# Kernel optimization log

Hardware: AMD Instinct MI355X
Metric: run time of the kernel (lower is better)

Reference implementation:

```python
import jax, jax.numpy as jnp
import numpy as np

B, N, E = 32, 1024, 16384
F_IN, H, C = 4, 4, 64
HC = H * C          # 256, concat head dim
FC0, FC1 = 128, 1
NEG_SLOPE = 0.2


def setup_inputs() -> dict:
    key = jax.random.key(0)
    ks = jax.random.split(key, 20)
    x = jax.random.normal(ks[0], (B, N, F_IN), dtype=jnp.float32)
    e = jax.random.normal(ks[1], (B, E, 1), dtype=jnp.float32)  # ignored by GATConv (edge_dim=None)
    edge_index0 = jax.random.randint(ks[2], (2, E), 0, N, dtype=jnp.int64)
    edge_index1 = jax.random.randint(ks[3], (2, E), 0, N, dtype=jnp.int64)

    def glorot(k, shape):
        fan = shape[0] + shape[-1]
        return jax.random.uniform(k, shape, jnp.float32, -1.0, 1.0) * np.sqrt(6.0 / fan)

    # GAT layer 0: F_IN -> (H, C)
    W0 = glorot(ks[4], (F_IN, HC))
    att_src0 = glorot(ks[5], (H, C))
    att_dst0 = glorot(ks[6], (H, C))
    b0 = jnp.zeros((HC,), jnp.float32)
    # GAT layer 1: HC -> (H, C)
    W1 = glorot(ks[7], (HC, HC))
    att_src1 = glorot(ks[8], (H, C))
    att_dst1 = glorot(ks[9], (H, C))
    b1 = jnp.zeros((HC,), jnp.float32)
    # FC head: 256 -> 128 -> ReLU -> 1 (no final ReLU: duplicate 'ReLU' module name)
    fc0_w = glorot(ks[10], (HC, FC0))
    fc0_b = jnp.zeros((FC0,), jnp.float32)
    fc1_w = glorot(ks[11], (FC0, FC1))
    fc1_b = jnp.zeros((FC1,), jnp.float32)
    return dict(x=x, e=e, edge_index0=edge_index0, edge_index1=edge_index1,
                W0=W0, att_src0=att_src0, att_dst0=att_dst0, b0=b0,
                W1=W1, att_src1=att_src1, att_dst1=att_dst1, b1=b1,
                fc0_w=fc0_w, fc0_b=fc0_b, fc1_w=fc1_w, fc1_b=fc1_b)


def _segment_softmax(logits, seg, num_segments):
    # softmax over edges grouped by target node, per head
    m = jax.ops.segment_max(logits, seg, num_segments=num_segments)
    m = jnp.where(jnp.isfinite(m), m, 0.0)
    ex = jnp.exp(logits - m[seg])
    s = jax.ops.segment_sum(ex, seg, num_segments=num_segments)
    return ex / (s[seg] + 1e-16)


def _gat_layer(xi, edge_index, W, att_src, att_dst, bias):
    # xi: (N, F_in); PyG GATConv, concat=True, add_self_loops=False
    h = (xi @ W).reshape(N, H, C)                 # (N, H, C)
    a_src = jnp.sum(h * att_src, axis=-1)         # (N, H)
    a_dst = jnp.sum(h * att_dst, axis=-1)         # (N, H)
    src, dst = edge_index[0], edge_index[1]       # message flows src -> dst
    alpha = jax.nn.leaky_relu(a_src[src] + a_dst[dst], NEG_SLOPE)  # (E, H)
    alpha = _segment_softmax(alpha, dst, N)
    msg = h[src] * alpha[:, :, None]              # (E, H, C)
    out = jax.ops.segment_sum(msg, dst, num_segments=N)  # (N, H, C)
    return out.reshape(N, HC) + bias


def reference(x, e, edge_index0, edge_index1,
              W0, att_src0, att_dst0, b0,
              W1, att_src1, att_dst1, b1,
              fc0_w, fc0_b, fc1_w, fc1_b):
    # edge_attr e is ignored (GATConv edge_dim=None), matching the original module
    def single(xi):
        y = _gat_layer(xi, edge_index0, W0, att_src0, att_dst0, b0)
        y = y + _gat_layer(y, edge_index1, W1, att_src1, att_dst1, b1)  # residual
        y = jax.nn.relu(y @ fc0_w + fc0_b)
        y = y @ fc1_w + fc1_b   # no final ReLU (duplicate module name in Sequential)
        return y                # (N, 1)
    return jax.vmap(single)(x)  # (B, N, 1)
```

## Files before the change

### kernel.cpp

```cpp
#include <hip/hip_runtime.h>

#define BB 32
#define NN 1024
#define EE 16384
#define NEG 0.2f

__device__ __forceinline__ float4 f4(float v) { return make_float4(v, v, v, v); }
__device__ __forceinline__ float4 f4max(float4 a, float4 b) {
    return make_float4(fmaxf(a.x, b.x), fmaxf(a.y, b.y), fmaxf(a.z, b.z), fmaxf(a.w, b.w));
}
__device__ __forceinline__ float4 f4add(float4 a, float4 b) {
    return make_float4(a.x + b.x, a.y + b.y, a.z + b.z, a.w + b.w);
}
__device__ __forceinline__ float4 f4sub(float4 a, float4 b) {
    return make_float4(a.x - b.x, a.y - b.y, a.z - b.z, a.w - b.w);
}
__device__ __forceinline__ float4 f4mul(float4 a, float4 b) {
    return make_float4(a.x * b.x, a.y * b.y, a.z * b.z, a.w * b.w);
}
__device__ __forceinline__ float4 f4exp(float4 a) {
    return make_float4(__expf(a.x), __expf(a.y), __expf(a.z), __expf(a.w));
}
__device__ __forceinline__ float4 shflx4(float4 v, int o) {
    return make_float4(__shfl_xor(v.x, o), __shfl_xor(v.y, o),
                       __shfl_xor(v.z, o), __shfl_xor(v.w, o));
}
__device__ __forceinline__ float4 leaky4(float4 z) {
    return make_float4(z.x > 0.f ? z.x : NEG * z.x, z.y > 0.f ? z.y : NEG * z.y,
                       z.z > 0.f ? z.z : NEG * z.z, z.w > 0.f ? z.w : NEG * z.w);
}

__global__ __launch_bounds__(1024) void k_csr_prep1(
    const int* __restrict__ ei0, const int* __restrict__ ei1,
    int* __restrict__ csr, int* __restrict__ off,
    const float* __restrict__ W0, const float* __restrict__ W1,
    const float* __restrict__ atts0, const float* __restrict__ attd0,
    const float* __restrict__ atts1, const float* __restrict__ attd1,
    float* __restrict__ ws1g, float* __restrict__ wd1g,
    float* __restrict__ ws0g, float* __restrict__ wd0g,
    float* __restrict__ Ug) {
    int blk = blockIdx.x, t = threadIdx.x;
    if (blk < 2) {
        __shared__ int cntS[NN];
        __shared__ int tmpS[NN];
        const int* ei = blk ? ei1 : ei0;
        int* o = off + blk * (NN + 1);
        int* c = csr + (blk << 14);
        cntS[t] = 0;
        __syncthreads();
        for (int e = t; e < EE; e += 1024) atomicAdd(&cntS[ei[EE + e]], 1);
        __syncthreads();
        int v0 = cntS[t];
        tmpS[t] = v0;
        __syncthreads();
        for (int d = 1; d < NN; d <<= 1) {
            int v = (t >= d) ? tmpS[t - d] : 0;
            __syncthreads();
            tmpS[t] += v;
            __syncthreads();
        }
        int excl = tmpS[t] - v0;
        o[t] = excl;
        if (t == NN - 1) o[NN] = tmpS[t];
        cntS[t] = excl;
        __syncthreads();
        for (int e = t; e < EE; e += 1024) {
            int d = ei[EE + e];
            int p = atomicAdd(&cntS[d], 1);
            c[p] = ei[e];
        }
        return;
    }
    int gid = ((blk - 2) << 10) + t;
    if (gid < 4096) {
        int i = gid >> 8, tt = gid & 255;
        int hp = i >> 2, f = i & 3;
        float a = 0.f;
        for (int c = 0; c < 64; ++c)
            a += W0[f * 256 + hp * 64 + c] * W1[(hp * 64 + c) * 256 + tt];
        Ug[i * 256 + tt] = a;
    } else if (gid < 5120) {
        int q = gid - 4096;
        int tt = q >> 2, h = q & 3;
        float a = 0.f;
        for (int c = 0; c < 64; ++c)
            a += W1[tt * 256 + h * 64 + c] * atts1[h * 64 + c];
        ws1g[q] = a;
    } else if (gid < 6144) {
        int q = gid - 5120;
        int tt = q >> 2, h = q & 3;
        float a = 0.f;
        for (int c = 0; c < 64; ++c)
            a += W1[tt * 256 + h * 64 + c] * attd1[h * 64 + c];
        wd1g[q] = a;
    } else if (gid < 6176) {
        int q = gid - 6144;
        int sel = q >> 4, i = q & 15;
        int f = i >> 2, h = i & 3;
        const float* att = sel ? attd0 : atts0;
        float a = 0.f;
        for (int c = 0; c < 64; ++c)
            a += W0[f * 256 + h * 64 + c] * att[h * 64 + c];
        (sel ? wd0g : ws0g)[i] = a;
    }
}

__global__ __launch_bounds__(512) void k_prep2(
    const float* __restrict__ W0, const float* __restrict__ W1,
    const float* __restrict__ b0, const float* __restrict__ ws1g,
    const float* __restrict__ wd1g, float* __restrict__ Msg,
    float* __restrict__ Mdg, float* __restrict__ csg, float* __restrict__ cdg,
    float* __restrict__ bbw1) {
    int t = threadIdx.x;
    if (t < 64) {
        int i = t >> 2, h = t & 3;
        int hp = i >> 2, f = i & 3;
        float a = 0.f;
        for (int c = 0; c < 64; ++c)
            a += W0[f * 256 + hp * 64 + c] * ws1g[(hp * 64 + c) * 4 + h];
        Msg[t] = a;
    } else if (t < 128) {
        int q = t - 64;
        int i = q >> 2, h = q & 3;
        int hp = i >> 2, f = i & 3;
        float a = 0.f;
        for (int c = 0; c < 64; ++c)
            a += W0[f * 256 + hp * 64 + c] * wd1g[(hp * 64 + c) * 4 + h];
        Mdg[q] = a;
    } else if (t < 132) {
        int h = t - 128;
        float a = 0.f;
        for (int tt = 0; tt < 256; ++tt) a += b0[tt] * ws1g[tt * 4 + h];
        csg[h] = a;
    } else if (t < 136) {
        int h = t - 132;
        float a = 0.f;
        for (int tt = 0; tt < 256; ++tt) a += b0[tt] * wd1g[tt * 4 + h];
        cdg[h] = a;
    } else if (t >= 256) {
        int tt = t - 256;
        float a = 0.f;
        for (int tp = 0; tp < 256; ++tp) a += b0[tp] * W1[tp * 256 + tt];
        bbw1[tt] = a;
    }
}

__global__ __launch_bounds__(256) void k_agg0_prepB(
    const float* __restrict__ x, const int* __restrict__ off,
    const int* __restrict__ csr, const float* __restrict__ ws0g,
    const float* __restrict__ wd0g, const float* __restrict__ Msg,
    const float* __restrict__ Mdg, const float* __restrict__ csg,
    const float* __restrict__ cdg, float* __restrict__ xbar,
    float* __restrict__ as1, float* __restrict__ ad1,
    const float* __restrict__ W0, const float* __restrict__ fc0w,
    const float* __restrict__ fc0b, const float* __restrict__ b0,
    const float* __restrict__ b1, const float* __restrict__ bbw1,
    const float* __restrict__ Ug, float* __restrict__ Wcat,
    float* __restrict__ c2a, float* __restrict__ c2b) {
    int blk = blockIdx.x, t = threadIdx.x;
    if (blk >= 2048) {
        int gid = ((blk - 2048) << 8) + t;
        if (gid < 8192) {
            int row = gid >> 7, u = gid & 127;
            int h = row >> 4, j = row & 15;
            float a = 0.f;
            for (int c = 0; c < 64; ++c)
                a += Ug[j * 256 + h * 64 + c] * fc0w[(h * 64 + c) * 128 + u];
            Wcat[row * 128 + u] = a;
        } else if (gid < 10240) {
            int row = gid >> 7, u = gid & 127;
            int j = row - 64;
            int h = j >> 2, f = j & 3;
            float a = 0.f;
            for (int c = 0; c < 64; ++c)
                a += W0[f * 256 + h * 64 + c] * fc0w[(h * 64 + c) * 128 + u];
            Wcat[row * 128 + u] = a;
        } else if (gid < 10368) {
            int u = gid - 10240;
            float a = fc0b[u];
            for (int tt = 0; tt < 256; ++tt)
                a += (b1[tt] + b0[tt]) * fc0w[tt * 128 + u];
            c2a[u] = a;
        } else if (gid < 10496) {
            int u = gid - 10368;
            float a = 0.f;
            for (int tt = 0; tt < 256; ++tt) a += bbw1[tt] * fc0w[tt * 128 + u];
            c2b[u] = a;
        }
        return;
    }
    int g = t >> 4, l = t & 15;
    int bn = (blk << 4) + g;
    int b = bn >> 10, n = bn & (NN - 1);
    int beg = off[n], end = off[n + 1];
    float ws[16], wd[16];
#pragma unroll
    for (int i = 0; i < 16; ++i) {
        ws[i] = ws0g[i];
        wd[i] = wd0g[i];
    }
    float4 xd = *(const float4*)&x[bn << 2];
    float4 adv;
    adv.x = xd.x * wd[0] + xd.y * wd[4] + xd.z * wd[8] + xd.w * wd[12];
    adv.y = xd.x * wd[1] + xd.y * wd[5] + xd.z * wd[9] + xd.w * wd[13];
    adv.z = xd.x * wd[2] + xd.y * wd[6] + xd.z * wd[10] + xd.w * wd[14];
    adv.w = xd.x * wd[3] + xd.y * wd[7] + xd.z * wd[11] + xd.w * wd[15];
    float4 m4 = f4(-1e30f), den = f4(0.f);
    float pacc[16];
#pragma unroll
    for (int i = 0; i < 16; ++i) pacc[i] = 0.f;
    for (int base = beg + l; base < end; base += 16) {
        int s = csr[base];
        float4 xs = *(const float4*)&x[((b << 10) + s) << 2];
        float4 av;
        av.x = xs.x * ws[0] + xs.y * ws[4] + xs.z * ws[8] + xs.w * ws[12];
        av.y = xs.x * ws[1] + xs.y * ws[5] + xs.z * ws[9] + xs.w * ws[13];
        av.z = xs.x * ws[2] + xs.y * ws[6] + xs.z * ws[10] + xs.w * ws[14];
        av.w = xs.x * ws[3] + xs.y * ws[7] + xs.z * ws[11] + xs.w * ws[15];
        float4 lv = leaky4(f4add(av, adv));
        float4 nm = f4max(m4, lv);
        float4 r = f4exp(f4sub(m4, nm));
        float4 ex = f4exp(f4sub(lv, nm));
        m4 = nm;
        den = f4add(f4mul(den, r), ex);
        float rr[4] = {r.x, r.y, r.z, r.w};
        float exa[4] = {ex.x, ex.y, ex.z, ex.w};
        float xsa[4] = {xs.x, xs.y, xs.z, xs.w};
#pragma unroll
        for (int i = 0; i < 16; ++i)
            pacc[i] = pacc[i] * rr[i >> 2] + exa[i >> 2] * xsa[i & 3];
    }
    float4 ml = m4;
#pragma unroll
    for (int o = 8; o; o >>= 1) m4 = f4max(m4, shflx4(m4, o));
    float4 sc = f4exp(f4sub(ml, m4));
    den = f4mul(den, sc);
    float sca[4] = {sc.x, sc.y, sc.z, sc.w};
#pragma unroll
    for (int i = 0; i < 16; ++i) pacc[i] *= sca[i >> 2];
#pragma unroll
    for (int o = 8; o; o >>= 1) {
        den = f4add(den, shflx4(den, o));
#pragma unroll
        for (int i = 0; i < 16; ++i) pacc[i] += __shfl_xor(pacc[i], o);
    }
    float iva[4] = {1.f / (den.x + 1e-16f), 1.f / (den.y + 1e-16f),
                    1.f / (den.z + 1e-16f), 1.f / (den.w + 1e-16f)};
    float xbn[16];
#pragma unroll
    for (int i = 0; i < 16; ++i) xbn[i] = pacc[i] * iva[i >> 2];
    if (l == 0) {
#pragma unroll
        for (int q = 0; q < 4; ++q) {
            float4 v = make_float4(xbn[q * 4], xbn[q * 4 + 1], xbn[q * 4 + 2],
                                   xbn[q * 4 + 3]);
            *(float4*)&xbar[(bn << 4) + (q << 2)] = v;
        }
    }
    if (l < 8) {
        int h = l & 3, sel = l >> 2;
        const float* M = sel ? Mdg : Msg;
        float a = sel ? cdg[h] : csg[h];
#pragma unroll
        for (int i = 0; i < 16; ++i) a += xbn[i] * M[i * 4 + h];
        (sel ? ad1 : as1)[(bn << 2) + h] = a;
    }
}

__global__ __launch_bounds__(256) void k_agg1(
    const float* __restrict__ xbar, const float* __restrict__ as1,
    const float* __restrict__ ad1, const int* __restrict__ off,
    const int* __restrict__ csr, float* __restrict__ xb2) {
    int t = threadIdx.x;
    int g = t >> 4, l = t & 15;
    int bn = (blockIdx.x << 4) + g;
    int b = bn >> 10, n = bn & (NN - 1);
    int beg = off[n], end = off[n + 1];
    float4 adv = *(const float4*)&ad1[bn << 2];
    float4 m4 = f4(-1e30f), den = f4(0.f);
    float pacc[64];
#pragma unroll
    for (int i = 0; i < 64; ++i) pacc[i] = 0.f;
    const float* xbb = xbar + ((size_t)b << 14);
    for (int base = beg + l; base < end; base += 16) {
        int s = csr[base];
        float4 av = *(const float4*)&as1[(((b << 10) + s)) << 2];
        float4 lv = leaky4(f4add(av, adv));
        float4 nm = f4max(m4, lv);
        float4 r = f4exp(f4sub(m4, nm));
        float4 ex = f4exp(f4sub(lv, nm));
        m4 = nm;
        den = f4add(f4mul(den, r), ex);
        const float* xp = xbb + (s << 4);
        float4 x0 = *(const float4*)(xp);
        float4 x1 = *(const float4*)(xp + 4);
        float4 x2 = *(const float4*)(xp + 8);
        float4 x3 = *(const float4*)(xp + 12);
        float rr[4] = {r.x, r.y, r.z, r.w};
        float exa[4] = {ex.x, ex.y, ex.z, ex.w};
        float xsa[16] = {x0.x, x0.y, x0.z, x0.w, x1.x, x1.y, x1.z, x1.w,
                         x2.x, x2.y, x2.z, x2.w, x3.x, x3.y, x3.z, x3.w};
#pragma unroll
        for (int h = 0; h < 4; ++h)
#pragma unroll
            for (int f = 0; f < 16; ++f)
                pacc[h * 16 + f] = pacc[h * 16 + f] * rr[h] + exa[h] * xsa[f];
    }
    float4 ml = m4;
#pragma unroll
    for (int o = 8; o; o >>= 1) m4 = f4max(m4, shflx4(m4, o));
    float4 sc = f4exp(f4sub(ml, m4));
    den = f4mul(den, sc);
    float sca[4] = {sc.x, sc.y, sc.z, sc.w};
#pragma unroll
    for (int i = 0; i < 64; ++i) pacc[i] *= sca[i >> 4];
#pragma unroll
    for (int o = 8; o; o >>= 1) {
        den = f4add(den, shflx4(den, o));
#pragma unroll
        for (int i = 0; i < 64; ++i) pacc[i] += __shfl_xor(pacc[i], o);
    }
    if (l == 0) {
        float iva[4] = {1.f / (den.x + 1e-16f), 1.f / (den.y + 1e-16f),
                        1.f / (den.z + 1e-16f), 1.f / (den.w + 1e-16f)};
#pragma unroll
        for (int q = 0; q < 16; ++q) {
            float iv = iva[q >> 2];
            float4 v = make_float4(pacc[q * 4] * iv, pacc[q * 4 + 1] * iv,
                                   pacc[q * 4 + 2] * iv, pacc[q * 4 + 3] * iv);
            *(float4*)&xb2[(bn << 6) + (q << 2)] = v;
        }
    }
}

#define AP 132
__global__ __launch_bounds__(256) void k_final(
    const float* __restrict__ xbar, const float* __restrict__ xb2,
    const float* __restrict__ Wcat, const float* __restrict__ c2a,
    const float* __restrict__ c2b, const float* __restrict__ fc1w,
    const float* __restrict__ fc1b, const int* __restrict__ off1,
    float* __restrict__ out) {
    __shared__ float Bs[80 * 128];
    __shared__ float As[80 * AP];
    __shared__ float c2as[128], c2bs[128], f1s[128];
    int t = threadIdx.x;
    int nb0 = blockIdx.x << 7;
    for (int i = t; i < 2560; i += 256) {
        float4 v = *(const float4*)&Wcat[i << 2];
        *(float4*)&Bs[i << 2] = v;
    }
    if (t < 128) {
        c2as[t] = c2a[t];
        c2bs[t] = c2b[t];
        f1s[t] = fc1w[t];
    }
#pragma unroll
    for (int i = 0; i < 8; ++i) {
        int q = t + (i << 8);
        int node = q >> 4, kq = q & 15;
        float4 v = *(const float4*)&xb2[((nb0 + node) << 6) + (kq << 2)];
        As[(kq * 4 + 0) * AP + node] = v.x;
        As[(kq * 4 + 1) * AP + node] = v.y;
        As[(kq * 4 + 2) * AP + node] = v.z;
        As[(kq * 4 + 3) * AP + node] = v.w;
    }
#pragma unroll
    for (int i = 0; i < 2; ++i) {
        int q = t + (i << 8);
        int node = q >> 2, kq = q & 3;
        float4 v = *(const float4*)&xbar[((nb0 + node) << 4) + (kq << 2)];
        As[(64 + kq * 4 + 0) * AP + node] = v.x;
        As[(64 + kq * 4 + 1) * AP + node] = v.y;
        As[(64 + kq * 4 + 2) * AP + node] = v.z;
        As[(64 + kq * 4 + 3) * AP + node] = v.w;
    }
    __syncthreads();
    int tx = t & 15, ty = t >> 4;
    int u0 = tx << 3, n0 = ty << 3;
    float za[8][8];
#pragma unroll
    for (int i = 0; i < 8; ++i)
#pragma unroll
        for (int j = 0; j < 8; ++j) za[i][j] = 0.f;
#pragma unroll 4
    for (int k = 0; k < 80; ++k) {
        float4 alo = *(const float4*)&As[k * AP + n0];
        float4 ahi = *(const float4*)&As[k * AP + n0 + 4];
        float4 blo = *(const float4*)&Bs[(k << 7) + u0];
        float4 bhi = *(const float4*)&Bs[(k << 7) + u0 + 4];
        float aa[8] = {alo.x, alo.y, alo.z, alo.w, ahi.x, ahi.y, ahi.z, ahi.w};
        float bb[8] = {blo.x, blo.y, blo.z, blo.w, bhi.x, bhi.y, bhi.z, bhi.w};
#pragma unroll
        for (int i = 0; i < 8; ++i)
#pragma unroll
            for (int j = 0; j < 8; ++j) za[i][j] += aa[i] * bb[j];
    }
    float fb = fc1b[0];
#pragma unroll
    for (int i = 0; i < 8; ++i) {
        int bnn = nb0 + n0 + i;
        int nl = bnn & (NN - 1);
        int deg = off1[nl + 1] - off1[nl];
        float part = 0.f;
#pragma unroll
        for (int j = 0; j < 8; ++j) {
            int u = u0 + j;
            float z = za[i][j] + c2as[u] + (deg > 0 ? c2bs[u] : 0.f);
            z = z > 0.f ? z : 0.f;
            part += z * f1s[u];
        }
#pragma unroll
        for (int o = 8; o; o >>= 1) part += __shfl_xor(part, o);
        if (tx == 0) out[bnn] = part + fb;
    }
}

extern "C" void kernel_launch(void* const* d_in, const int* in_sizes, int n_in,
                              void* d_out, int out_size, void* d_ws, size_t ws_size,
                              hipStream_t stream) {
    const float* x = (const float*)d_in[0];
    const int* ei0 = (const int*)d_in[2];
    const int* ei1 = (const int*)d_in[3];
    const float* W0 = (const float*)d_in[4];
    const float* atts0 = (const float*)d_in[5];
    const float* attd0 = (const float*)d_in[6];
    const float* b0 = (const float*)d_in[7];
    const float* W1 = (const float*)d_in[8];
    const float* atts1 = (const float*)d_in[9];
    const float* attd1 = (const float*)d_in[10];
    const float* b1 = (const float*)d_in[11];
    const float* fc0w = (const float*)d_in[12];
    const float* fc0b = (const float*)d_in[13];
    const float* fc1w = (const float*)d_in[14];
    const float* fc1b = (const float*)d_in[15];
    float* out = (float*)d_out;

    float* fw = (float*)d_ws;
    float* xbar = fw;                 fw += (size_t)BB * NN * 16;
    float* xb2 = fw;                  fw += (size_t)BB * NN * 64;
    float* as1 = fw;                  fw += (size_t)BB * NN * 4;
    float* ad1 = fw;                  fw += (size_t)BB * NN * 4;
    float* Ug = fw;                   fw += 4096;
    float* Wcat = fw;                 fw += 80 * 128;
    float* bbw1 = fw;                 fw += 256;
    float* c2a = fw;                  fw += 128;
    float* c2b = fw;                  fw += 128;
    float* ws0g = fw;                 fw += 16;
    float* wd0g = fw;                 fw += 16;
    float* Msg = fw;                  fw += 64;
    float* Mdg = fw;                  fw += 64;
    float* csg = fw;                  fw += 4;
    float* cdg = fw;                  fw += 4;
    float* ws1g = fw;                 fw += 1024;
    float* wd1g = fw;                 fw += 1024;
    int* ip = (int*)fw;
    int* off = ip;                    ip += 2 * (NN + 1);
    int* csr = ip;

    k_csr_prep1<<<9, 1024, 0, stream>>>(ei0, ei1, csr, off, W0, W1, atts0,
                                        attd0, atts1, attd1, ws1g, wd1g, ws0g,
                                        wd0g, Ug);
    k_prep2<<<1, 512, 0, stream>>>(W0, W1, b0, ws1g, wd1g, Msg, Mdg, csg, cdg,
                                   bbw1);
    k_agg0_prepB<<<2089, 256, 0, stream>>>(
        x, off, csr, ws0g, wd0g, Msg, Mdg, csg, cdg, xbar, as1, ad1, W0, fc0w,
        fc0b, b0, b1, bbw1, Ug, Wcat, c2a, c2b);
    k_agg1<<<BB * NN / 16, 256, 0, stream>>>(xbar, as1, ad1, off + (NN + 1),
                                             csr + EE, xb2);
    k_final<<<BB * NN / 128, 256, 0, stream>>>(xbar, xb2, Wcat, c2a, c2b, fc1w,
                                               fc1b, off + (NN + 1), out);
}
```

Before: 182.1 us.

## Split CSR build into parallel count, scan and scatter kernels

```diff
diff --git a/kernel.cpp b/kernel.cpp
--- a/kernel.cpp
+++ b/kernel.cpp
@@ -30,48 +30,23 @@
                        z.z > 0.f ? z.z : NEG * z.z, z.w > 0.f ? z.w : NEG * z.w);
 }
 
-__global__ __launch_bounds__(1024) void k_csr_prep1(
+__global__ __launch_bounds__(256) void k_count_prep1(
     const int* __restrict__ ei0, const int* __restrict__ ei1,
-    int* __restrict__ csr, int* __restrict__ off,
-    const float* __restrict__ W0, const float* __restrict__ W1,
-    const float* __restrict__ atts0, const float* __restrict__ attd0,
-    const float* __restrict__ atts1, const float* __restrict__ attd1,
-    float* __restrict__ ws1g, float* __restrict__ wd1g,
-    float* __restrict__ ws0g, float* __restrict__ wd0g,
-    float* __restrict__ Ug) {
+    int* __restrict__ cnt, const float* __restrict__ W0,
+    const float* __restrict__ W1, const float* __restrict__ atts0,
+    const float* __restrict__ attd0, const float* __restrict__ atts1,
+    const float* __restrict__ attd1, float* __restrict__ ws1g,
+    float* __restrict__ wd1g, float* __restrict__ ws0g,
+    float* __restrict__ wd0g, float* __restrict__ Ug) {
     int blk = blockIdx.x, t = threadIdx.x;
-    if (blk < 2) {
-        __shared__ int cntS[NN];
-        __shared__ int tmpS[NN];
-        const int* ei = blk ? ei1 : ei0;
-        int* o = off + blk * (NN + 1);
-        int* c = csr + (blk << 14);
-        cntS[t] = 0;
-        __syncthreads();
-        for (int e = t; e < EE; e += 1024) atomicAdd(&cntS[ei[EE + e]], 1);
-        __syncthreads();
-        int v0 = cntS[t];
-        tmpS[t] = v0;
-        __syncthreads();
-        for (int d = 1; d < NN; d <<= 1) {
-            int v = (t >= d) ? tmpS[t - d] : 0;
-            __syncthreads();
-            tmpS[t] += v;
-            __syncthreads();
-        }
-        int excl = tmpS[t] - v0;
-        o[t] = excl;
-        if (t == NN - 1) o[NN] = tmpS[t];
-        cntS[t] = excl;
-        __syncthreads();
-        for (int e = t; e < EE; e += 1024) {
-            int d = ei[EE + e];
-            int p = atomicAdd(&cntS[d], 1);
-            c[p] = ei[e];
-        }
+    if (blk < 128) {
+        int list = blk >> 6;
+        int e = ((blk & 63) << 8) + t;
+        const int* ei = list ? ei1 : ei0;
+        atomicAdd(&cnt[(list << 10) + ei[EE + e]], 1);
         return;
     }
-    int gid = ((blk - 2) << 10) + t;
+    int gid = ((blk - 128) << 8) + t;
     if (gid < 4096) {
         int i = gid >> 8, tt = gid & 255;
         int hp = i >> 2, f = i & 3;
@@ -105,44 +80,79 @@
     }
 }
 
-__global__ __launch_bounds__(512) void k_prep2(
+__global__ __launch_bounds__(1024) void k_scan_prep2(
+    int* __restrict__ cnt, int* __restrict__ off,
     const float* __restrict__ W0, const float* __restrict__ W1,
     const float* __restrict__ b0, const float* __restrict__ ws1g,
     const float* __restrict__ wd1g, float* __restrict__ Msg,
     float* __restrict__ Mdg, float* __restrict__ csg, float* __restrict__ cdg,
     float* __restrict__ bbw1) {
-    int t = threadIdx.x;
-    if (t < 64) {
-        int i = t >> 2, h = t & 3;
-        int hp = i >> 2, f = i & 3;
+    int blk = blockIdx.x, t = threadIdx.x;
+    if (blk < 2) {
+        __shared__ int s[NN];
+        int* c = cnt + (blk << 10);
+        int* o = off + blk * (NN + 1);
+        int v0 = c[t];
+        s[t] = v0;
+        __syncthreads();
+        for (int d = 1; d < NN; d <<= 1) {
+            int v = (t >= d) ? s[t - d] : 0;
+            __syncthreads();
+            s[t] += v;
+            __syncthreads();
+        }
+        int excl = s[t] - v0;
+        o[t] = excl;
+        c[t] = excl;
+        if (t == NN - 1) o[NN] = s[NN - 1];
+        return;
+    }
+    if (blk == 2) {
+        if (t < 64) {
+            int i = t >> 2, h = t & 3;
+            int hp = i >> 2, f = i & 3;
+            float a = 0.f;
+            for (int c = 0; c < 64; ++c)
+                a += W0[f * 256 + hp * 64 + c] * ws1g[(hp * 64 + c) * 4 + h];
+            Msg[t] = a;
+        } else if (t < 128) {
+            int q = t - 64;
+            int i = q >> 2, h = q & 3;
+            int hp = i >> 2, f = i & 3;
+            float a = 0.f;
+            for (int c = 0; c < 64; ++c)
+                a += W0[f * 256 + hp * 64 + c] * wd1g[(hp * 64 + c) * 4 + h];
+            Mdg[q] = a;
+        } else if (t < 132) {
+            int h = t - 128;
+            float a = 0.f;
+            for (int tt = 0; tt < 256; ++tt) a += b0[tt] * ws1g[tt * 4 + h];
+            csg[h] = a;
+        } else if (t < 136) {
+            int h = t - 132;
+            float a = 0.f;
+            for (int tt = 0; tt < 256; ++tt) a += b0[tt] * wd1g[tt * 4 + h];
+            cdg[h] = a;
+        }
+        return;
+    }
+    if (t < 256) {
         float a = 0.f;
-        for (int c = 0; c < 64; ++c)
-            a += W0[f * 256 + hp * 64 + c] * ws1g[(hp * 64 + c) * 4 + h];
-        Msg[t] = a;
-    } else if (t < 128) {
-        int q = t - 64;
-        int i = q >> 2, h = q & 3;
-        int hp = i >> 2, f = i & 3;
-        float a = 0.f;
-        for (int c = 0; c < 64; ++c)
-            a += W0[f * 256 + hp * 64 + c] * wd1g[(hp * 64 + c) * 4 + h];
-        Mdg[q] = a;
-    } else if (t < 132) {
-        int h = t - 128;
-        float a = 0.f;
-        for (int tt = 0; tt < 256; ++tt) a += b0[tt] * ws1g[tt * 4 + h];
-        csg[h] = a;
-    } else if (t < 136) {
-        int h = t - 132;
-        float a = 0.f;
-        for (int tt = 0; tt < 256; ++tt) a += b0[tt] * wd1g[tt * 4 + h];
-        cdg[h] = a;
-    } else if (t >= 256) {
-        int tt = t - 256;
-        float a = 0.f;
-        for (int tp = 0; tp < 256; ++tp) a += b0[tp] * W1[tp * 256 + tt];
-        bbw1[tt] = a;
-    }
+        for (int tp = 0; tp < 256; ++tp) a += b0[tp] * W1[tp * 256 + t];
+        bbw1[t] = a;
+    }
+}
+
+__global__ __launch_bounds__(256) void k_scatter(
+    const int* __restrict__ ei0, const int* __restrict__ ei1,
+    int* __restrict__ cur, int* __restrict__ csr) {
+    int list = blockIdx.x >> 6;
+    int e = ((blockIdx.x & 63) << 8) + threadIdx.x;
+    const int* ei = list ? ei1 : ei0;
+    int sv = ei[e];
+    int d = ei[EE + e];
+    int p = atomicAdd(&cur[(list << 10) + d], 1);
+    csr[(list << 14) + p] = sv;
 }
 
 __global__ __launch_bounds__(256) void k_agg0_prepB(
@@ -455,13 +465,16 @@
     float* wd1g = fw;                 fw += 1024;
     int* ip = (int*)fw;
     int* off = ip;                    ip += 2 * (NN + 1);
+    int* cnt = ip;                    ip += 2 * NN;
     int* csr = ip;
 
-    k_csr_prep1<<<9, 1024, 0, stream>>>(ei0, ei1, csr, off, W0, W1, atts0,
-                                        attd0, atts1, attd1, ws1g, wd1g, ws0g,
-                                        wd0g, Ug);
-    k_prep2<<<1, 512, 0, stream>>>(W0, W1, b0, ws1g, wd1g, Msg, Mdg, csg, cdg,
-                                   bbw1);
+    hipMemsetAsync(cnt, 0, 2 * NN * sizeof(int), stream);
+    k_count_prep1<<<153, 256, 0, stream>>>(ei0, ei1, cnt, W0, W1, atts0, attd0,
+                                           atts1, attd1, ws1g, wd1g, ws0g,
+                                           wd0g, Ug);
+    k_scan_prep2<<<4, 1024, 0, stream>>>(cnt, off, W0, W1, b0, ws1g, wd1g,
+                                         Msg, Mdg, csg, cdg, bbw1);
+    k_scatter<<<128, 256, 0, stream>>>(ei0, ei1, cnt, csr);
     k_agg0_prepB<<<2089, 256, 0, stream>>>(
         x, off, csr, ws0g, wd0g, Msg, Mdg, csg, cdg, xbar, as1, ad1, W0, fc0w,
         fc0b, b0, b1, bbw1, Ug, Wcat, c2a, c2b);
```

New measurement: 174.3 us. -4.3%, faster.
